# Kernel optimization log

Measured on AMD Instinct MI355X. Metric: run time of the kernel, lower is better.

Reference implementation:

```python
import jax, jax.numpy as jnp
import numpy as np

# static architecture constants
NUM_GRAPHS = 64
NODES_PER_GRAPH = 512
N_TOTAL = NUM_GRAPHS * NODES_PER_GRAPH          # 32768
AVG_DEG = 16
E_TOTAL = N_TOTAL * AVG_DEG                      # 524288
NODE_NUMBER = 1000
EMB = 128
DIMF = 128
NUM_LAYERS = 4
K = 64
DIM_TARGET = 2
LATENT = NUM_LAYERS * DIMF + 1                   # 513


def setup_inputs() -> dict:
    key = jax.random.key(0)
    ks = jax.random.split(key, 16)
    # node ids
    x = jax.random.randint(ks[0], (N_TOTAL,), 0, NODE_NUMBER, dtype=jnp.int32)
    # edges confined within each graph
    epg = NODES_PER_GRAPH * AVG_DEG
    src_l = jax.random.randint(ks[1], (NUM_GRAPHS, epg), 0, NODES_PER_GRAPH, dtype=jnp.int32)
    dst_l = jax.random.randint(ks[2], (NUM_GRAPHS, epg), 0, NODES_PER_GRAPH, dtype=jnp.int32)
    off = (jnp.arange(NUM_GRAPHS, dtype=jnp.int32) * NODES_PER_GRAPH)[:, None]
    edge_index = jnp.stack([(src_l + off).reshape(-1), (dst_l + off).reshape(-1)])  # [2,E]
    batch = jnp.repeat(jnp.arange(NUM_GRAPHS, dtype=jnp.int32), NODES_PER_GRAPH)

    def lin(k, fi, fo):
        return jax.random.normal(k, (fi, fo), jnp.float32) / np.sqrt(fi)

    emb = jax.random.normal(ks[3], (NODE_NUMBER, EMB), jnp.float32)
    W_convs = jnp.stack([lin(jax.random.fold_in(ks[4], l), EMB if l == 0 else DIMF, DIMF)
                         for l in range(NUM_LAYERS)])            # [L,128,128]
    b_convs = jnp.zeros((NUM_LAYERS, DIMF), jnp.float32)
    W_last = lin(ks[5], DIMF, 1)
    b_last = jnp.zeros((1,), jnp.float32)
    conv1_w = jax.random.normal(ks[6], (16, 1, LATENT), jnp.float32) / np.sqrt(LATENT)
    conv1_b = jnp.zeros((16,), jnp.float32)
    conv2_w = jax.random.normal(ks[7], (32, 16, 5), jnp.float32) / np.sqrt(16 * 5)
    conv2_b = jnp.zeros((32,), jnp.float32)
    dd = (K - 2) // 2 + 1                      # 32
    in_dense = (dd - 5 + 1) * 32               # 896
    d1_w = lin(ks[8], in_dense, dd)
    d1_b = jnp.zeros((dd,), jnp.float32)
    d2_w = lin(ks[9], dd, DIM_TARGET)
    d2_b = jnp.zeros((DIM_TARGET,), jnp.float32)
    return dict(x=x, edge_index=edge_index, batch=batch, emb=emb,
                W_convs=W_convs, b_convs=b_convs, W_last=W_last, b_last=b_last,
                conv1_w=conv1_w, conv1_b=conv1_b, conv2_w=conv2_w, conv2_b=conv2_b,
                d1_w=d1_w, d1_b=d1_b, d2_w=d2_w, d2_b=d2_b)


def _gcn(h, W, b, src, dst, norm):
    # linear -> gather -> degree-normalize -> scatter-add (DGCNNConv with aggr='add')
    h = h @ W + b
    msg = h[src] * norm[:, None]
    return jax.ops.segment_sum(msg, dst, num_segments=N_TOTAL)


def reference(x, edge_index, batch, emb, W_convs, b_convs, W_last, b_last,
              conv1_w, conv1_b, conv2_w, conv2_b, d1_w, d1_b, d2_w, d2_b):
    loops = jnp.arange(N_TOTAL, dtype=edge_index.dtype)
    src = jnp.concatenate([edge_index[0], loops])
    dst = jnp.concatenate([edge_index[1], loops])
    # deg = degree(src); norm = deg^-1 gathered at dst (as in DGCNNConv.message)
    deg = jax.ops.segment_sum(jnp.ones_like(src, jnp.float32), src, num_segments=N_TOTAL)
    norm = (1.0 / deg)[dst]

    h = emb[x]                                           # [N,128]
    hidden = []
    for l in range(NUM_LAYERS):
        h = jnp.tanh(_gcn(h, W_convs[l], b_convs[l], src, dst, norm))
        hidden.append(h)
    h = jnp.tanh(_gcn(h, W_last, b_last, src, dst, norm))  # [N,1]
    hidden.append(h)
    xcat = jnp.concatenate(hidden, axis=1)               # [N, 513]

    # global_sort_pool: batch is sorted with equal-size graphs -> dense reshape
    x3 = xcat.reshape(NUM_GRAPHS, NODES_PER_GRAPH, LATENT)
    order = jnp.argsort(-x3[..., -1], axis=1)[:, :K]     # descending by last channel, top-k
    pooled = jnp.take_along_axis(x3, order[:, :, None], axis=1)  # [B,K,513]

    # conv1d(1,16,kernel=513,stride=513) over [B,1,K*513] == per-row projection
    y1 = jax.nn.relu(jnp.einsum('bkd,od->bok', pooled, conv1_w[:, 0, :])
                     + conv1_b[None, :, None])           # [B,16,K]
    L = K // 2
    y1 = y1.reshape(NUM_GRAPHS, 16, L, 2).max(axis=-1)   # maxpool(2,2)
    y2 = jax.lax.conv_general_dilated(y1, conv2_w, (1,), 'VALID',
                                      dimension_numbers=('NCH', 'OIH', 'NCH'))
    y2 = jax.nn.relu(y2 + conv2_b[None, :, None])        # [B,32,L-4]
    flat = y2.reshape(NUM_GRAPHS, -1)                    # [B,896]
    h1 = jax.nn.relu(flat @ d1_w + d1_b)                 # dropout is identity in eval
    logits = h1 @ d2_w + d2_b
    return jax.nn.softmax(logits, axis=-1)
```

## Files before the change

### kernel.cpp

```cpp
#include <hip/hip_runtime.h>
#include <hip/hip_bf16.h>
#include <math.h>

#define N_TOTAL 32768
#define E_TOTAL 524288
#define NUM_GRAPHS 64
#define NPG 512
#define MAXD 64
#define KTOP 64
#define LATENT 513
#define PPAD 524

typedef __attribute__((ext_vector_type(8))) short bf16x8;
typedef __attribute__((ext_vector_type(4))) float f32x4;

__device__ __forceinline__ unsigned short f2bf(float f) {
    unsigned u = __float_as_uint(f);
    return (unsigned short)((u + 0x7FFFu + ((u >> 16) & 1u)) >> 16);
}
__device__ __forceinline__ float bf2f(unsigned short h) {
    return __uint_as_float(((unsigned)h) << 16);
}
__device__ __forceinline__ int swz(int bir, int row) {
    return (bir & ~127) | ((bir & 127) ^ ((row & 7) << 4));
}


__global__ __launch_bounds__(256) void k_init(int* __restrict__ deg, int* __restrict__ cnt) {
    int i = blockIdx.x * 256 + threadIdx.x;
    if (i < N_TOTAL) { deg[i] = 1; cnt[i] = 0; }
}

__global__ __launch_bounds__(256) void k_zero(int4* __restrict__ p) {
    p[(size_t)blockIdx.x * 256 + threadIdx.x] = make_int4(0, 0, 0, 0);
}

__global__ __launch_bounds__(256) void k_build(const int* __restrict__ ei,
                                               int* __restrict__ deg, int* __restrict__ cnt,
                                               int* __restrict__ adj, unsigned* __restrict__ Au) {
    int e = blockIdx.x * 256 + threadIdx.x;
    if (e >= E_TOTAL) return;
    int s = ei[e];
    int d = ei[E_TOTAL + e];
    atomicAdd(&deg[s], 1);
    int slot = atomicAdd(&cnt[d], 1);
    if (slot < MAXD) adj[(size_t)d * MAXD + slot] = s;
    int g = d >> 9, v = d & 511, u = s & 511;
    atomicAdd(&Au[((size_t)g << 17) + (v << 8) + (u >> 1)], 1u << ((u & 1) << 4));
}

__global__ __launch_bounds__(256) void k_convA(const unsigned* __restrict__ Au,
                                               unsigned short* __restrict__ Asw) {
    size_t idx = (size_t)blockIdx.x * 256 + threadIdx.x;
    size_t b4 = idx * 4;
    int g = (int)(b4 >> 17);
    int rem = (int)(b4 & 131071);
    int v = rem >> 8;
    int u0 = (rem & 255) * 2;
    uint4 cw = *(const uint4*)(Au + b4);
    unsigned r[4];
#pragma unroll
    for (int i = 0; i < 4; ++i) {
        unsigned wv = (&cw.x)[i];
        int ua = u0 + 2 * i, ub = ua + 1;
        float ca = (float)(wv & 0xFFFFu) + ((ua == v) ? 1.f : 0.f);
        float cb = (float)(wv >> 16)     + ((ub == v) ? 1.f : 0.f);
        r[i] = (unsigned)f2bf(ca) | ((unsigned)f2bf(cb) << 16);
    }
    *(int4*)(Asw + ((size_t)g * 512 + v) * 512 + u0) = make_int4(r[0], r[1], r[2], r[3]);
}

__global__ __launch_bounds__(256) void k_prep(const float* __restrict__ Wc,
                                              unsigned short* __restrict__ Wth,
                                              unsigned short* __restrict__ Wtl) {
    __shared__ float tile[64][65];
    int b = blockIdx.x;
    int l = b >> 2, t = b & 3;
    int k0 = (t >> 1) * 64, o0 = (t & 1) * 64;
    int lane = threadIdx.x & 63, q = threadIdx.x >> 6;
    const float* Wsrc = Wc + (size_t)l * 16384;
#pragma unroll
    for (int it = 0; it < 16; ++it) {
        int r = it * 4 + q;
        tile[r][lane] = Wsrc[(size_t)(k0 + r) * 128 + o0 + lane];
    }
    __syncthreads();
#pragma unroll
    for (int it = 0; it < 16; ++it) {
        int o = it * 4 + q;
        float v = tile[lane][o];
        unsigned short h = f2bf(v);
        unsigned short lo = f2bf(v - bf2f(h));
        size_t dst = (size_t)l * 16384 + (size_t)(o0 + o) * 128 + k0 + lane;
        Wth[dst] = h; Wtl[dst] = lo;
    }
}

__global__ __launch_bounds__(256) void k_embT(const int* __restrict__ x,
                                              const float* __restrict__ emb,
                                              unsigned short* __restrict__ Ph,
                                              unsigned short* __restrict__ Pl) {
    __shared__ float P[64][132];
    __shared__ int nodes[64];
    int b = blockIdx.x;
    int g = b >> 3, ck = b & 7;
    int tid = threadIdx.x;
    if (tid < 64) nodes[tid] = x[g * NPG + ck * 64 + tid];
    __syncthreads();
#pragma unroll
    for (int c = 0; c < 8; ++c) {
        int idx = tid + c * 256;
        int row = idx >> 5, c4 = idx & 31;
        float4 vv = *(const float4*)(emb + (size_t)nodes[row] * 128 + c4 * 4);
        *(float4*)&P[row][c4 * 4] = vv;
    }
    __syncthreads();
#pragma unroll
    for (int c = 0; c < 4; ++c) {
        int idx = tid + c * 256;
        int ch = idx >> 3, grp = idx & 7;
        unsigned hw[4], lw[4];
#pragma unroll
        for (int j = 0; j < 4; ++j) {
            float a  = P[grp * 8 + 2 * j][ch];
            float bq = P[grp * 8 + 2 * j + 1][ch];
            unsigned short ha = f2bf(a),  hb = f2bf(bq);
            unsigned short la = f2bf(a - bf2f(ha)), lb = f2bf(bq - bf2f(hb));
            hw[j] = (unsigned)ha | ((unsigned)hb << 16);
            lw[j] = (unsigned)la | ((unsigned)lb << 16);
        }
        size_t base = ((size_t)g * 128 + ch) * 512 + ck * 64 + grp * 8;
        *(int4*)(Ph + base) = make_int4(hw[0], hw[1], hw[2], hw[3]);
        *(int4*)(Pl + base) = make_int4(lw[0], lw[1], lw[2], lw[3]);
    }
}


__global__ __launch_bounds__(256) void k_layer(const unsigned short* __restrict__ Ph,
                                               const unsigned short* __restrict__ Pl,
                                               const unsigned short* __restrict__ Asw,
                                               const unsigned short* __restrict__ Wth,
                                               const unsigned short* __restrict__ Wtl,
                                               const float* __restrict__ bvec,
                                               const float* __restrict__ Wl,
                                               const float* __restrict__ bl,
                                               float* __restrict__ tmp,
                                               float* __restrict__ Hout,
                                               unsigned short* __restrict__ Poh,
                                               unsigned short* __restrict__ Pol,
                                               const int* __restrict__ cnt,
                                               const int* __restrict__ deg) {
    __shared__ char lds[40960];
    int tid = threadIdx.x;
    int w = tid >> 6, lane = tid & 63;
    int bid = blockIdx.x;
    int g = (bid & 7) * 8 + ((bid >> 3) & 7);
    int vblk = bid >> 6;
    int nodebase = g * NPG + vblk * 64;
    int r = lane & 15, kb = lane >> 4;

    f32x4 acc[8];
#pragma unroll
    for (int n = 0; n < 8; ++n) acc[n] = (f32x4){0.f, 0.f, 0.f, 0.f};
    size_t Abase = ((size_t)(g * NPG + vblk * 64)) * 512;
    int vrow = w * 16 + r;

    for (int kt = 0; kt < 8; ++kt) {
#pragma unroll
        for (int c = 0; c < 10; ++c) {
            int idx = tid + c * 256;
            const unsigned short* src;
            int row, off16, ldsbase;
            if (idx < 512)       { row = idx >> 3;          off16 = idx & 7;
                src = Asw + Abase + (size_t)row * 512 + kt * 64 + off16 * 8;
                ldsbase = 0; }
            else if (idx < 1536) { int j = idx - 512;  row = j >> 3; off16 = j & 7;
                src = Ph + ((size_t)g * 128 + row) * 512 + kt * 64 + off16 * 8;
                ldsbase = 8192; }
            else                 { int j = idx - 1536; row = j >> 3; off16 = j & 7;
                src = Pl + ((size_t)g * 128 + row) * 512 + kt * 64 + off16 * 8;
                ldsbase = 24576; }
            int4 v = *(const int4*)src;
            *(int4*)(lds + ldsbase + row * 128 + swz(off16 * 16, row)) = v;
        }
        __syncthreads();
#pragma unroll
        for (int s2 = 0; s2 < 2; ++s2) {
            int bir = s2 * 64 + kb * 16;
            bf16x8 aA = *(const bf16x8*)(lds + vrow * 128 + swz(bir, vrow));
#pragma unroll
            for (int n = 0; n < 8; ++n) {
                int ch = n * 16 + r;
                bf16x8 bh = *(const bf16x8*)(lds + 8192  + ch * 128 + swz(bir, ch));
                bf16x8 bl2 = *(const bf16x8*)(lds + 24576 + ch * 128 + swz(bir, ch));
                acc[n] = __builtin_amdgcn_mfma_f32_16x16x32_bf16(aA, bh,  acc[n], 0, 0, 0);
                acc[n] = __builtin_amdgcn_mfma_f32_16x16x32_bf16(aA, bl2, acc[n], 0, 0, 0);
            }
        }
        __syncthreads();
    }

#pragma unroll
    for (int n = 0; n < 8; ++n) {
#pragma unroll
        for (int q = 0; q < 4; ++q) {
            int v64 = w * 16 + kb * 4 + q;
            int ch = n * 16 + r;
            float s = acc[n][q];
            unsigned short h = f2bf(s), lo = f2bf(s - bf2f(h));
            int addr = v64 * 256 + swz(ch * 2, v64);
            *(unsigned short*)(lds + 8192 + addr)  = h;
            *(unsigned short*)(lds + 24576 + addr) = lo;
        }
    }
    __syncthreads();

    int rowbase = nodebase + w * 16;
    bf16x8 ah[4], al[4];
#pragma unroll
    for (int ks = 0; ks < 4; ++ks) {
        int v64 = w * 16 + r;
        int addr = v64 * 256 + swz(ks * 64 + kb * 16, v64);
        ah[ks] = *(const bf16x8*)(lds + 8192 + addr);
        al[ks] = *(const bf16x8*)(lds + 24576 + addr);
    }
    float invd[4], cp1[4];
#pragma unroll
    for (int q = 0; q < 4; ++q) {
        int nd = rowbase + kb * 4 + q;
        invd[q] = 1.0f / (float)deg[nd];
        cp1[q]  = (float)(cnt[nd] + 1);
    }
    float z[4] = {0.f, 0.f, 0.f, 0.f};
    unsigned hiW[8][2], loW[8][2];
#pragma unroll
    for (int ct = 0; ct < 8; ++ct) {
        const unsigned short* Wh = Wth + (size_t)(ct * 16 + r) * 128;
        const unsigned short* Wo = Wtl + (size_t)(ct * 16 + r) * 128;
        f32x4 a = {0.f, 0.f, 0.f, 0.f};
#pragma unroll
        for (int ks = 0; ks < 4; ++ks) {
            bf16x8 wh = *(const bf16x8*)(Wh + ks * 32 + kb * 8);
            bf16x8 wl = *(const bf16x8*)(Wo + ks * 32 + kb * 8);
            a = __builtin_amdgcn_mfma_f32_16x16x32_bf16(ah[ks], wh, a, 0, 0, 0);
            a = __builtin_amdgcn_mfma_f32_16x16x32_bf16(ah[ks], wl, a, 0, 0, 0);
            a = __builtin_amdgcn_mfma_f32_16x16x32_bf16(al[ks], wh, a, 0, 0, 0);
        }
        float bcol = bvec[ct * 16 + r];
        float wlast = Wl ? Wl[ct * 16 + r] : 0.f;
        unsigned short hq[4], lq[4];
#pragma unroll
        for (int q = 0; q < 4; ++q) {
            float val = tanhf((a[q] + bcol * cp1[q]) * invd[q]);
            Hout[(size_t)(rowbase + kb * 4 + q) * 128 + ct * 16 + r] = val;
            z[q] = fmaf(val, wlast, z[q]);
            hq[q] = f2bf(val);
            lq[q] = f2bf(val - bf2f(hq[q]));
        }
        hiW[ct][0] = (unsigned)hq[0] | ((unsigned)hq[1] << 16);
        hiW[ct][1] = (unsigned)hq[2] | ((unsigned)hq[3] << 16);
        loW[ct][0] = (unsigned)lq[0] | ((unsigned)lq[1] << 16);
        loW[ct][1] = (unsigned)lq[2] | ((unsigned)lq[3] << 16);
    }

    if (Poh) {
        __syncthreads();
#pragma unroll
        for (int ct = 0; ct < 8; ++ct) {
            int o = ct * 16 + r;
            int v64 = w * 16 + kb * 4;
            int addr = o * 128 + swz(v64 * 2, o);
            *(int2*)(lds + addr)         = make_int2(hiW[ct][0], hiW[ct][1]);
            *(int2*)(lds + 16384 + addr) = make_int2(loW[ct][0], loW[ct][1]);
        }
        __syncthreads();
#pragma unroll
        for (int c = 0; c < 8; ++c) {
            int idx = tid + c * 256;
            int arr = idx >> 10;
            int j = idx & 1023;
            int o = j >> 3, off16 = j & 7;
            int4 v = *(const int4*)(lds + arr * 16384 + o * 128 + swz(off16 * 16, o));
            unsigned short* dst = (arr ? Pol : Poh) + ((size_t)g * 128 + o) * 512 + vblk * 64 + off16 * 8;
            *(int4*)dst = v;
        }
    }

    if (Wl) {
#pragma unroll
        for (int m = 1; m < 16; m <<= 1) {
            z[0] += __shfl_xor(z[0], m); z[1] += __shfl_xor(z[1], m);
            z[2] += __shfl_xor(z[2], m); z[3] += __shfl_xor(z[3], m);
        }
        if (r == 0) {
            float b0 = bl[0];
#pragma unroll
            for (int q = 0; q < 4; ++q) tmp[rowbase + kb * 4 + q] = z[q] + b0;
        }
    }
}


__global__ __launch_bounds__(256) void k_sort(const float* __restrict__ tmp,
                                              const int* __restrict__ adj,
                                              const int* __restrict__ cnt,
                                              const int* __restrict__ deg,
                                              float* __restrict__ lastc,
                                              int* __restrict__ topk) {
    __shared__ float v[512];
    __shared__ int ix[512];
    int g = blockIdx.x, tid = threadIdx.x;
    for (int i = tid; i < 512; i += 256) {
        int node = g * NPG + i;
        float s = tmp[node];
        int c = cnt[node]; if (c > MAXD) c = MAXD;
        const int* av = adj + (size_t)node * MAXD;
#pragma unroll 4
        for (int q = 0; q < c; ++q) s += tmp[av[q]];
        float val = tanhf(s / (float)deg[node]);
        lastc[node] = val;
        v[i] = val; ix[i] = i;
    }
    __syncthreads();
    for (int ksz = 2; ksz <= 512; ksz <<= 1) {
        for (int jj = ksz >> 1; jj > 0; jj >>= 1) {
            for (int i = tid; i < 512; i += 256) {
                int p = i ^ jj;
                if (p > i) {
                    float va = v[i], vb = v[p];
                    int ia = ix[i], ib = ix[p];
                    bool b_before_a = (vb > va) || (vb == va && ib < ia);
                    bool up = (i & ksz) == 0;
                    bool sw = up ? b_before_a : !b_before_a;
                    if (sw) { v[i] = vb; v[p] = va; ix[i] = ib; ix[p] = ia; }
                }
            }
            __syncthreads();
        }
    }
    for (int k = tid; k < KTOP; k += 256) topk[g * KTOP + k] = g * NPG + ix[k];
}


__global__ __launch_bounds__(256) void k_conv1(const int* __restrict__ topk,
                                               const float* __restrict__ h0,
                                               const float* __restrict__ h1,
                                               const float* __restrict__ h2,
                                               const float* __restrict__ h3,
                                               const float* __restrict__ lastc,
                                               const float* __restrict__ c1w,
                                               const float* __restrict__ c1b,
                                               float* __restrict__ y1p) {
    __shared__ float P[16][PPAD];
    __shared__ float Y1c[16][16];
    __shared__ int nodes[16];
    int bid = blockIdx.x;
    int g = bid >> 2, cc = bid & 3;
    int tid = threadIdx.x;
    if (tid < 16) nodes[tid] = topk[g * KTOP + cc * 16 + tid];
    __syncthreads();
    {
        int r = tid >> 4, t4 = tid & 15;
        int node = nodes[r];
#pragma unroll
        for (int jj = 0; jj < 8; ++jj) {
            int d = (t4 + 16 * jj) * 4;
            const float* src = (d < 128) ? h0 : (d < 256) ? h1 : (d < 384) ? h2 : h3;
            float4 val = *(const float4*)(src + (size_t)node * 128 + (d & 127));
            *(float4*)&P[r][d] = val;
        }
        if (t4 == 0) P[r][512] = lastc[node];
    }
    __syncthreads();
    int o = tid >> 4, kk = tid & 15;
    const float* w = c1w + (size_t)o * LATENT;
    float a0 = 0.f, a1 = 0.f, a2 = 0.f, a3 = 0.f;
    for (int d = 0; d < 512; d += 4) {
        float4 p = *(const float4*)&P[kk][d];
        a0 = fmaf(p.x, w[d],     a0);
        a1 = fmaf(p.y, w[d + 1], a1);
        a2 = fmaf(p.z, w[d + 2], a2);
        a3 = fmaf(p.w, w[d + 3], a3);
    }
    float s = ((a0 + a1) + (a2 + a3)) + P[kk][512] * w[512] + c1b[o];
    Y1c[o][kk] = fmaxf(s, 0.f);
    __syncthreads();
    if (tid < 128) {
        int oo = tid >> 3, l = tid & 7;
        y1p[(size_t)g * 512 + oo * 32 + cc * 8 + l] = fmaxf(Y1c[oo][2 * l], Y1c[oo][2 * l + 1]);
    }
}


__global__ __launch_bounds__(256) void k_tail(const float* __restrict__ y1p,
                                              const float* __restrict__ c2w, const float* __restrict__ c2b,
                                              const float* __restrict__ d1w, const float* __restrict__ d1b,
                                              const float* __restrict__ d2w, const float* __restrict__ d2b,
                                              float* __restrict__ out) {
    __shared__ float Y1P[16][32];
    __shared__ float Y2[32][28];
    __shared__ float H1s[32];
    __shared__ float red[256];
    int g = blockIdx.x, tid = threadIdx.x;
    for (int t = tid; t < 512; t += 256) ((float*)Y1P)[t] = y1p[(size_t)g * 512 + t];
    __syncthreads();
    for (int t = tid; t < 32 * 28; t += 256) {
        int o2 = t / 28, tt = t - o2 * 28;
        float s = c2b[o2];
#pragma unroll
        for (int i = 0; i < 16; ++i)
#pragma unroll
            for (int dt = 0; dt < 5; ++dt)
                s = fmaf(Y1P[i][tt + dt], c2w[o2 * 80 + i * 5 + dt], s);
        Y2[o2][tt] = fmaxf(s, 0.f);
    }
    __syncthreads();
    {
        int jcol = tid >> 3, part = tid & 7;
        float s = 0.f;
        for (int rr = 0; rr < 4; ++rr) {
            int o2 = part * 4 + rr;
            int base = o2 * 28;
            for (int tt = 0; tt < 28; ++tt)
                s = fmaf(Y2[o2][tt], d1w[(size_t)(base + tt) * 32 + jcol], s);
        }
        red[tid] = s;
        __syncthreads();
        if (part == 0) {
            float t = 0.f;
#pragma unroll
            for (int p = 0; p < 8; ++p) t += red[tid + p];
            H1s[jcol] = fmaxf(t + d1b[jcol], 0.f);
        }
        __syncthreads();
    }
    if (tid == 0) {
        float l0 = d2b[0], l1 = d2b[1];
        for (int jc = 0; jc < 32; ++jc) {
            l0 = fmaf(H1s[jc], d2w[jc * 2 + 0], l0);
            l1 = fmaf(H1s[jc], d2w[jc * 2 + 1], l1);
        }
        float m = fmaxf(l0, l1);
        float e0 = expf(l0 - m), e1 = expf(l1 - m);
        float inv = 1.f / (e0 + e1);
        out[g * 2 + 0] = e0 * inv;
        out[g * 2 + 1] = e1 * inv;
    }
}


extern "C" void kernel_launch(void* const* d_in, const int* in_sizes, int n_in,
                              void* d_out, int out_size, void* d_ws, size_t ws_size,
                              hipStream_t stream) {
    const int*   x    = (const int*)d_in[0];
    const int*   ei   = (const int*)d_in[1];
    const float* emb  = (const float*)d_in[3];
    const float* Wc   = (const float*)d_in[4];
    const float* bc   = (const float*)d_in[5];
    const float* Wl   = (const float*)d_in[6];
    const float* bl   = (const float*)d_in[7];
    const float* c1w  = (const float*)d_in[8];
    const float* c1b  = (const float*)d_in[9];
    const float* c2w  = (const float*)d_in[10];
    const float* c2b  = (const float*)d_in[11];
    const float* d1w  = (const float*)d_in[12];
    const float* d1b  = (const float*)d_in[13];
    const float* d2w  = (const float*)d_in[14];
    const float* d2b  = (const float*)d_in[15];
    float* out = (float*)d_out;

    char* ws = (char*)d_ws;
    int*   deg  = (int*)ws;            ws += (size_t)N_TOTAL * 4;
    int*   cnt  = (int*)ws;            ws += (size_t)N_TOTAL * 4;
    int*   adj  = (int*)ws;            ws += (size_t)N_TOTAL * MAXD * 4;
    float* Hid0 = (float*)ws;          ws += (size_t)N_TOTAL * 128 * 4;
    float* Hid1 = (float*)ws;          ws += (size_t)N_TOTAL * 128 * 4;
    float* Hid2 = (float*)ws;          ws += (size_t)N_TOTAL * 128 * 4;
    float* Hid3 = (float*)ws;          ws += (size_t)N_TOTAL * 128 * 4;
    unsigned short* Wth = (unsigned short*)ws;  ws += (size_t)4 * 128 * 128 * 2;
    unsigned short* Wtl = (unsigned short*)ws;  ws += (size_t)4 * 128 * 128 * 2;
    float* tmp  = (float*)ws;          ws += (size_t)N_TOTAL * 4;
    float* lastc= (float*)ws;          ws += (size_t)N_TOTAL * 4;
    int*   topk = (int*)ws;            ws += (size_t)NUM_GRAPHS * KTOP * 4;
    float* y1p  = (float*)ws;          ws += (size_t)NUM_GRAPHS * 16 * 32 * 4;
    unsigned* Au = (unsigned*)ws;      ws += (size_t)NUM_GRAPHS * 512 * 256 * 4;
    unsigned short* Asw = (unsigned short*)ws;  ws += (size_t)NUM_GRAPHS * 512 * 512 * 2;
    unsigned short* PAh = (unsigned short*)ws;  ws += (size_t)NUM_GRAPHS * 128 * 512 * 2;
    unsigned short* PAl = (unsigned short*)ws;  ws += (size_t)NUM_GRAPHS * 128 * 512 * 2;
    unsigned short* PBh = (unsigned short*)ws;  ws += (size_t)NUM_GRAPHS * 128 * 512 * 2;
    unsigned short* PBl = (unsigned short*)ws;  ws += (size_t)NUM_GRAPHS * 128 * 512 * 2;

    k_init <<<N_TOTAL / 256, 256, 0, stream>>>(deg, cnt);
    k_zero <<<8192, 256, 0, stream>>>((int4*)Au);
    k_build<<<E_TOTAL / 256, 256, 0, stream>>>(ei, deg, cnt, adj, Au);
    k_prep <<<16, 256, 0, stream>>>(Wc, Wth, Wtl);
    k_convA<<<8192, 256, 0, stream>>>(Au, Asw);
    k_embT <<<NUM_GRAPHS * 8, 256, 0, stream>>>(x, emb, PAh, PAl);

    float* Hids[4] = {Hid0, Hid1, Hid2, Hid3};
    unsigned short* Pin_h[4] = {PAh, PBh, PAh, PBh};
    unsigned short* Pin_l[4] = {PAl, PBl, PAl, PBl};
    unsigned short* Pout_h[4] = {PBh, PAh, PBh, nullptr};
    unsigned short* Pout_l[4] = {PBl, PAl, PBl, nullptr};
    for (int l = 0; l < 4; ++l) {
        const float* wl  = (l == 3) ? Wl : nullptr;
        const float* blp = (l == 3) ? bl : nullptr;
        float*       tp  = (l == 3) ? tmp : nullptr;
        k_layer<<<512, 256, 0, stream>>>(Pin_h[l], Pin_l[l], Asw,
                                         Wth + (size_t)l * 16384, Wtl + (size_t)l * 16384,
                                         bc + (size_t)l * 128, wl, blp, tp,
                                         Hids[l], Pout_h[l], Pout_l[l], cnt, deg);
    }
    k_sort <<<NUM_GRAPHS, 256, 0, stream>>>(tmp, adj, cnt, deg, lastc, topk);
    k_conv1<<<NUM_GRAPHS * 4, 256, 0, stream>>>(topk, Hid0, Hid1, Hid2, Hid3, lastc, c1w, c1b, y1p);
    k_tail <<<NUM_GRAPHS, 256, 0, stream>>>(y1p, c2w, c2b, d1w, d1b, d2w, d2b, out);
}
```

Measured before the change: 407.0 us.

## Pack adjacency counts as 8-bit and load layer GEMM operands directly from global

The adjacency count buffer now packs multiplicities into 8-bit fields instead of 16-bit, which halves the zeroing and conversion traffic. The layer kernel drops the LDS staging and barriers for the aggregation GEMM and reads A and P fragments straight from global memory (relying on cache), which shrinks LDS use and may raise occupancy. The trade-offs are uncoalesced or redundant global loads across waves, and a risk of 8-bit count overflow if an edge multiplicity reaches 255 or more.

New measurement: 555.1 us. 1.36x slower.

```diff
diff --git a/kernel.cpp b/kernel.cpp
--- a/kernel.cpp
+++ b/kernel.cpp
@@ -46,28 +46,30 @@
     int slot = atomicAdd(&cnt[d], 1);
     if (slot < MAXD) adj[(size_t)d * MAXD + slot] = s;
     int g = d >> 9, v = d & 511, u = s & 511;
-    atomicAdd(&Au[((size_t)g << 17) + (v << 8) + (u >> 1)], 1u << ((u & 1) << 4));
+    size_t bidx = ((size_t)(g * 512 + v) << 9) + u;
+    atomicAdd(&Au[bidx >> 2], 1u << ((u & 3) << 3));
 }
 
 __global__ __launch_bounds__(256) void k_convA(const unsigned* __restrict__ Au,
                                                unsigned short* __restrict__ Asw) {
     size_t idx = (size_t)blockIdx.x * 256 + threadIdx.x;
-    size_t b4 = idx * 4;
-    int g = (int)(b4 >> 17);
-    int rem = (int)(b4 & 131071);
-    int v = rem >> 8;
-    int u0 = (rem & 255) * 2;
-    uint4 cw = *(const uint4*)(Au + b4);
+    int g = (int)(idx >> 15);
+    int rem = (int)(idx & 32767);
+    int v = rem >> 6;
+    int u0 = (rem & 63) * 8;
+    size_t ebase = ((size_t)(g * 512 + v) << 9) + u0;
+    uint2 cw = *(const uint2*)(Au + (ebase >> 2));
     unsigned r[4];
 #pragma unroll
     for (int i = 0; i < 4; ++i) {
-        unsigned wv = (&cw.x)[i];
+        unsigned wv = (i < 2) ? cw.x : cw.y;
+        int sh = (i & 1) * 16;
         int ua = u0 + 2 * i, ub = ua + 1;
-        float ca = (float)(wv & 0xFFFFu) + ((ua == v) ? 1.f : 0.f);
-        float cb = (float)(wv >> 16)     + ((ub == v) ? 1.f : 0.f);
+        float ca = (float)((wv >> sh) & 0xFFu)       + ((ua == v) ? 1.f : 0.f);
+        float cb = (float)((wv >> (sh + 8)) & 0xFFu) + ((ub == v) ? 1.f : 0.f);
         r[i] = (unsigned)f2bf(ca) | ((unsigned)f2bf(cb) << 16);
     }
-    *(int4*)(Asw + ((size_t)g * 512 + v) * 512 + u0) = make_int4(r[0], r[1], r[2], r[3]);
+    *(int4*)(Asw + ebase) = make_int4(r[0], r[1], r[2], r[3]);
 }
 
 __global__ __launch_bounds__(256) void k_prep(const float* __restrict__ Wc,
@@ -150,54 +152,36 @@
                                                unsigned short* __restrict__ Pol,
                                                const int* __restrict__ cnt,
                                                const int* __restrict__ deg) {
-    __shared__ char lds[40960];
+    __shared__ char lds[32768];
     int tid = threadIdx.x;
     int w = tid >> 6, lane = tid & 63;
     int bid = blockIdx.x;
     int g = (bid & 7) * 8 + ((bid >> 3) & 7);
     int vblk = bid >> 6;
     int nodebase = g * NPG + vblk * 64;
+    int rowbase = nodebase + w * 16;
     int r = lane & 15, kb = lane >> 4;
 
     f32x4 acc[8];
 #pragma unroll
     for (int n = 0; n < 8; ++n) acc[n] = (f32x4){0.f, 0.f, 0.f, 0.f};
-    size_t Abase = ((size_t)(g * NPG + vblk * 64)) * 512;
-    int vrow = w * 16 + r;
+    const unsigned short* Arow = Asw + (size_t)(rowbase + r) * 512;
+    const unsigned short* Pbh  = Ph + ((size_t)g * 128 + r) * 512;
+    const unsigned short* Pbl  = Pl + ((size_t)g * 128 + r) * 512;
 
     for (int kt = 0; kt < 8; ++kt) {
 #pragma unroll
-        for (int c = 0; c < 10; ++c) {
-            int idx = tid + c * 256;
-            const unsigned short* src;
-            int row, off16, ldsbase;
-            if (idx < 512)       { row = idx >> 3;          off16 = idx & 7;
-                src = Asw + Abase + (size_t)row * 512 + kt * 64 + off16 * 8;
-                ldsbase = 0; }
-            else if (idx < 1536) { int j = idx - 512;  row = j >> 3; off16 = j & 7;
-                src = Ph + ((size_t)g * 128 + row) * 512 + kt * 64 + off16 * 8;
-                ldsbase = 8192; }
-            else                 { int j = idx - 1536; row = j >> 3; off16 = j & 7;
-                src = Pl + ((size_t)g * 128 + row) * 512 + kt * 64 + off16 * 8;
-                ldsbase = 24576; }
-            int4 v = *(const int4*)src;
-            *(int4*)(lds + ldsbase + row * 128 + swz(off16 * 16, row)) = v;
-        }
-        __syncthreads();
-#pragma unroll
         for (int s2 = 0; s2 < 2; ++s2) {
-            int bir = s2 * 64 + kb * 16;
-            bf16x8 aA = *(const bf16x8*)(lds + vrow * 128 + swz(bir, vrow));
+            int ko = kt * 64 + s2 * 32 + kb * 8;
+            bf16x8 aA = *(const bf16x8*)(Arow + ko);
 #pragma unroll
             for (int n = 0; n < 8; ++n) {
-                int ch = n * 16 + r;
-                bf16x8 bh = *(const bf16x8*)(lds + 8192  + ch * 128 + swz(bir, ch));
-                bf16x8 bl2 = *(const bf16x8*)(lds + 24576 + ch * 128 + swz(bir, ch));
+                bf16x8 bh  = *(const bf16x8*)(Pbh + (size_t)n * 8192 + ko);
+                bf16x8 bl2 = *(const bf16x8*)(Pbl + (size_t)n * 8192 + ko);
                 acc[n] = __builtin_amdgcn_mfma_f32_16x16x32_bf16(aA, bh,  acc[n], 0, 0, 0);
                 acc[n] = __builtin_amdgcn_mfma_f32_16x16x32_bf16(aA, bl2, acc[n], 0, 0, 0);
             }
         }
-        __syncthreads();
     }
 
 #pragma unroll
@@ -209,20 +193,19 @@
             float s = acc[n][q];
             unsigned short h = f2bf(s), lo = f2bf(s - bf2f(h));
             int addr = v64 * 256 + swz(ch * 2, v64);
-            *(unsigned short*)(lds + 8192 + addr)  = h;
-            *(unsigned short*)(lds + 24576 + addr) = lo;
-        }
-    }
-    __syncthreads();
-
-    int rowbase = nodebase + w * 16;
+            *(unsigned short*)(lds + addr)         = h;
+            *(unsigned short*)(lds + 16384 + addr) = lo;
+        }
+    }
+    __syncthreads();
+
     bf16x8 ah[4], al[4];
 #pragma unroll
     for (int ks = 0; ks < 4; ++ks) {
         int v64 = w * 16 + r;
         int addr = v64 * 256 + swz(ks * 64 + kb * 16, v64);
-        ah[ks] = *(const bf16x8*)(lds + 8192 + addr);
-        al[ks] = *(const bf16x8*)(lds + 24576 + addr);
+        ah[ks] = *(const bf16x8*)(lds + addr);
+        al[ks] = *(const bf16x8*)(lds + 16384 + addr);
     }
     float invd[4], cp1[4];
 #pragma unroll
@@ -483,7 +466,7 @@
     float* lastc= (float*)ws;          ws += (size_t)N_TOTAL * 4;
     int*   topk = (int*)ws;            ws += (size_t)NUM_GRAPHS * KTOP * 4;
     float* y1p  = (float*)ws;          ws += (size_t)NUM_GRAPHS * 16 * 32 * 4;
-    unsigned* Au = (unsigned*)ws;      ws += (size_t)NUM_GRAPHS * 512 * 256 * 4;
+    unsigned* Au = (unsigned*)ws;      ws += (size_t)NUM_GRAPHS * 512 * 512;
     unsigned short* Asw = (unsigned short*)ws;  ws += (size_t)NUM_GRAPHS * 512 * 512 * 2;
     unsigned short* PAh = (unsigned short*)ws;  ws += (size_t)NUM_GRAPHS * 128 * 512 * 2;
     unsigned short* PAl = (unsigned short*)ws;  ws += (size_t)NUM_GRAPHS * 128 * 512 * 2;
@@ -491,7 +474,7 @@
     unsigned short* PBl = (unsigned short*)ws;  ws += (size_t)NUM_GRAPHS * 128 * 512 * 2;
 
     k_init <<<N_TOTAL / 256, 256, 0, stream>>>(deg, cnt);
-    k_zero <<<8192, 256, 0, stream>>>((int4*)Au);
+    k_zero <<<4096, 256, 0, stream>>>((int4*)Au);
     k_build<<<E_TOTAL / 256, 256, 0, stream>>>(ei, deg, cnt, adj, Au);
     k_prep <<<16, 256, 0, stream>>>(Wc, Wth, Wtl);
     k_convA<<<8192, 256, 0, stream>>>(Au, Asw);
```
